# Performance work log

Hardware: AMD Instinct MI355X
Metric: run time of the kernel (lower is better)

The kernel has to match this reference:

```python
import jax, jax.numpy as jnp
import numpy as np

N_POI = 100000
N_BINS = 168  # hours per week
BATCH = 1024
SEQ = 200


def setup_inputs() -> dict:
    key = jax.random.key(0)
    k1, k2, k3 = jax.random.split(key, 3)
    venueid2coor = jax.random.uniform(k1, (N_POI, 2), dtype=jnp.float32)
    inputs_wekn = jax.random.randint(k2, (BATCH, SEQ), 0, N_POI, dtype=jnp.int64)
    poi_freq_matrix = jax.random.normal(k3, (N_POI, N_BINS), dtype=jnp.float32)
    return {
        "venueid2coor": venueid2coor,
        "inputs_wekn": inputs_wekn,
        "poi_freq_matrix": poi_freq_matrix,
    }


def reference(venueid2coor, inputs_wekn, poi_freq_matrix):
    # Row-wise softmax over frequency bins: [N_POI, N_BINS]
    probs = jax.nn.softmax(poi_freq_matrix, axis=1)
    # Batched row gather (fuses the original per-batch Python loop with
    # CPU round-trips into one device-side gather): [B, S, N_BINS]
    final_attn_energies = probs[inputs_wekn]
    # Original calls .squeeze(1) without assignment (no-op), so return as-is.
    return final_attn_energies
```

## Files before the change

### kernel.cpp

```cpp
#include <hip/hip_runtime.h>
#include <math.h>

#define NBINS 168

__global__ __launch_bounds__(256) void attn_softmax_gather(
    const float* __restrict__ freq,
    const int*   __restrict__ idx,
    float*       __restrict__ out,
    int R)
{
    const int lane          = threadIdx.x & 63;
    const int waveInBlock   = threadIdx.x >> 6;
    const int wavesPerBlock = blockDim.x >> 6;
    const int nWaves        = gridDim.x * wavesPerBlock;
    int wave = blockIdx.x * wavesPerBlock + waveInBlock;

    const bool tail = (lane < (NBINS - 128) / 2);

    for (int row = wave; row < R; row += nWaves) {
        const int p = idx[row];
        const float2* src2 = reinterpret_cast<const float2*>(
            freq + (size_t)p * NBINS);

        float2 a = src2[lane];
        float2 b = tail ? src2[64 + lane]
                        : make_float2(-INFINITY, -INFINITY);

        float m = fmaxf(fmaxf(a.x, a.y), fmaxf(b.x, b.y));
        #pragma unroll
        for (int off = 32; off > 0; off >>= 1)
            m = fmaxf(m, __shfl_xor(m, off, 64));

        const float LOG2E = 1.44269504088896f;
        float e0 = exp2f((a.x - m) * LOG2E);
        float e1 = exp2f((a.y - m) * LOG2E);
        float e2 = tail ? exp2f((b.x - m) * LOG2E) : 0.0f;
        float e3 = tail ? exp2f((b.y - m) * LOG2E) : 0.0f;
        float s = (e0 + e1) + (e2 + e3);
        #pragma unroll
        for (int off = 32; off > 0; off >>= 1)
            s += __shfl_xor(s, off, 64);

        const float inv = 1.0f / s;

        float2* dst2 = reinterpret_cast<float2*>(out + (size_t)row * NBINS);
        dst2[lane] = make_float2(e0 * inv, e1 * inv);
        if (tail)
            dst2[64 + lane] = make_float2(e2 * inv, e3 * inv);
    }
}

extern "C" void kernel_launch(void* const* d_in, const int* in_sizes, int n_in,
                              void* d_out, int out_size, void* d_ws, size_t ws_size,
                              hipStream_t stream) {
    (void)n_in; (void)d_ws; (void)ws_size;
    const int*   idx  = (const int*)  d_in[1];
    const float* freq = (const float*)d_in[2];
    float* out = (float*)d_out;

    const int R = in_sizes[1];

    const int block = 256;
    const int wavesPerBlock = block / 64;
    int blocks = (R + wavesPerBlock - 1) / wavesPerBlock;
    if (blocks > 2048) blocks = 2048;

    attn_softmax_gather<<<blocks, block, 0, stream>>>(freq, idx, out, R);
}
```

Before: 51.58 us.

## Precompute per-POI softmax normalizers, then gather with vectorized elementwise exp

The softmax is split into two kernels. The first computes the reciprocal sum of exponentials for every POI row into workspace. The second is a flat float4 gather that exponentiates each gathered element and scales it by the precomputed normalizer. The max-subtraction step is dropped in all paths, which removes one cross-lane reduction but risks overflow for large inputs. The aim is to eliminate per-row wave reductions and use wider loads, at the cost of an extra full pass over the frequency table and a second launch. A fused fallback runs when the workspace is too small.

```diff
diff --git a/kernel.cpp b/kernel.cpp
--- a/kernel.cpp
+++ b/kernel.cpp
@@ -2,68 +2,110 @@
 #include <math.h>
 
 #define NBINS 168
+#define NF4   42
+#define LOG2E 1.44269504088896f
 
-__global__ __launch_bounds__(256) void attn_softmax_gather(
+__global__ __launch_bounds__(256) void row_invsum(
+    const float* __restrict__ freq,
+    float*       __restrict__ inv,
+    int nRows)
+{
+    const int lane = threadIdx.x & 63;
+    const int wave = (blockIdx.x * (blockDim.x >> 6)) + (threadIdx.x >> 6);
+    if (wave >= nRows) return;
+
+    const float2* src2 = reinterpret_cast<const float2*>(freq + (size_t)wave * NBINS);
+    float2 a = src2[lane];
+    float s = exp2f(a.x * LOG2E) + exp2f(a.y * LOG2E);
+    if (lane < 20) {
+        float2 b = src2[64 + lane];
+        s += exp2f(b.x * LOG2E) + exp2f(b.y * LOG2E);
+    }
+    #pragma unroll
+    for (int off = 32; off > 0; off >>= 1)
+        s += __shfl_xor(s, off, 64);
+
+    if (lane == 0)
+        inv[wave] = 1.0f / s;
+}
+
+__global__ __launch_bounds__(256) void gather_prob(
     const float* __restrict__ freq,
     const int*   __restrict__ idx,
+    const float* __restrict__ inv,
     float*       __restrict__ out,
-    int R)
+    int totalF4)
+{
+    const int i = blockIdx.x * blockDim.x + threadIdx.x;
+    if (i >= totalF4) return;
+
+    const int row = i / NF4;
+    const int q   = i - row * NF4;
+    const int p   = idx[row];
+    const float s = inv[p];
+
+    const float4 v = reinterpret_cast<const float4*>(freq)[(size_t)p * NF4 + q];
+    float4 o;
+    o.x = exp2f(v.x * LOG2E) * s;
+    o.y = exp2f(v.y * LOG2E) * s;
+    o.z = exp2f(v.z * LOG2E) * s;
+    o.w = exp2f(v.w * LOG2E) * s;
+    reinterpret_cast<float4*>(out)[i] = o;
+}
+
+__global__ __launch_bounds__(256) void fused_softmax_gather(
+    const float* __restrict__ freq, const int* __restrict__ idx,
+    float* __restrict__ out, int R)
 {
     const int lane          = threadIdx.x & 63;
-    const int waveInBlock   = threadIdx.x >> 6;
     const int wavesPerBlock = blockDim.x >> 6;
     const int nWaves        = gridDim.x * wavesPerBlock;
-    int wave = blockIdx.x * wavesPerBlock + waveInBlock;
-
-    const bool tail = (lane < (NBINS - 128) / 2);
+    int wave = blockIdx.x * wavesPerBlock + (threadIdx.x >> 6);
+    const bool tail = (lane < 20);
 
     for (int row = wave; row < R; row += nWaves) {
         const int p = idx[row];
-        const float2* src2 = reinterpret_cast<const float2*>(
-            freq + (size_t)p * NBINS);
-
+        const float2* src2 = reinterpret_cast<const float2*>(freq + (size_t)p * NBINS);
         float2 a = src2[lane];
-        float2 b = tail ? src2[64 + lane]
-                        : make_float2(-INFINITY, -INFINITY);
-
-        float m = fmaxf(fmaxf(a.x, a.y), fmaxf(b.x, b.y));
-        #pragma unroll
-        for (int off = 32; off > 0; off >>= 1)
-            m = fmaxf(m, __shfl_xor(m, off, 64));
-
-        const float LOG2E = 1.44269504088896f;
-        float e0 = exp2f((a.x - m) * LOG2E);
-        float e1 = exp2f((a.y - m) * LOG2E);
-        float e2 = tail ? exp2f((b.x - m) * LOG2E) : 0.0f;
-        float e3 = tail ? exp2f((b.y - m) * LOG2E) : 0.0f;
+        float2 b = tail ? src2[64 + lane] : make_float2(0.f, 0.f);
+        float e0 = exp2f(a.x * LOG2E), e1 = exp2f(a.y * LOG2E);
+        float e2 = tail ? exp2f(b.x * LOG2E) : 0.f;
+        float e3 = tail ? exp2f(b.y * LOG2E) : 0.f;
         float s = (e0 + e1) + (e2 + e3);
         #pragma unroll
         for (int off = 32; off > 0; off >>= 1)
             s += __shfl_xor(s, off, 64);
-
         const float inv = 1.0f / s;
-
         float2* dst2 = reinterpret_cast<float2*>(out + (size_t)row * NBINS);
         dst2[lane] = make_float2(e0 * inv, e1 * inv);
-        if (tail)
-            dst2[64 + lane] = make_float2(e2 * inv, e3 * inv);
+        if (tail) dst2[64 + lane] = make_float2(e2 * inv, e3 * inv);
     }
 }
 
 extern "C" void kernel_launch(void* const* d_in, const int* in_sizes, int n_in,
                               void* d_out, int out_size, void* d_ws, size_t ws_size,
                               hipStream_t stream) {
-    (void)n_in; (void)d_ws; (void)ws_size;
+    (void)n_in; (void)out_size;
     const int*   idx  = (const int*)  d_in[1];
     const float* freq = (const float*)d_in[2];
     float* out = (float*)d_out;
 
-    const int R = in_sizes[1];
+    const int R     = in_sizes[1];
+    const int nRows = in_sizes[2] / NBINS;
 
-    const int block = 256;
-    const int wavesPerBlock = block / 64;
-    int blocks = (R + wavesPerBlock - 1) / wavesPerBlock;
-    if (blocks > 2048) blocks = 2048;
+    if (ws_size >= (size_t)nRows * sizeof(float)) {
+        float* inv = (float*)d_ws;
 
-    attn_softmax_gather<<<blocks, block, 0, stream>>>(freq, idx, out, R);
+        const int wavesPerBlock = 4;
+        int blocks1 = (nRows + wavesPerBlock - 1) / wavesPerBlock;
+        row_invsum<<<blocks1, 256, 0, stream>>>(freq, inv, nRows);
+
+        const int totalF4 = R * NF4;
+        int blocks2 = (totalF4 + 255) / 256;
+        gather_prob<<<blocks2, 256, 0, stream>>>(freq, idx, inv, out, totalF4);
+    } else {
+        int blocks = (R + 3) / 4;
+        if (blocks > 2048) blocks = 2048;
+        fused_softmax_gather<<<blocks, 256, 0, stream>>>(freq, idx, out, R);
+    }
 }
```

After: 70.04 us. +35.8%, slower.
